# Kernel optimization log

Hardware: AMD Instinct MI355X
Metric: run time of the kernel (lower is better)

## Reference

```python
import jax, jax.numpy as jnp
import numpy as np

B, T, C = 4, 1024, 1024
H, HKV, D = 16, 4, 64
GATE_CH = 12
ROPE_THETA = 10000.0


def _rms_norm(x):
    # F.rms_norm with default eps = machine epsilon of dtype, no learnable scale
    eps = jnp.finfo(x.dtype).eps
    ms = jnp.mean(jnp.square(x), axis=-1, keepdims=True)
    return x * jax.lax.rsqrt(ms + eps)


def _apply_rotary(x, cos, sin):
    # x: (B, T, h, D); cos/sin: (1, T, 1, D//2). Half-split rotation.
    d = x.shape[-1] // 2
    x1, x2 = x[..., :d], x[..., d:]
    y1 = x1 * cos + x2 * sin
    y2 = -x1 * sin + x2 * cos
    return jnp.concatenate([y1, y2], axis=-1)


def setup_inputs() -> dict:
    key = jax.random.key(0)
    ks = jax.random.split(key, 8)
    x = jax.random.normal(ks[0], (B, T, C), dtype=jnp.float32)
    ve = jax.random.normal(ks[1], (B, T, HKV * D), dtype=jnp.float32)
    # real RoPE tables, shape (1, T, 1, D//2)
    half = D // 2
    inv_freq = 1.0 / (ROPE_THETA ** (np.arange(half, dtype=np.float32) / half))
    freqs = np.arange(T, dtype=np.float32)[:, None] * inv_freq[None, :]
    cos = jnp.asarray(np.cos(freqs), dtype=jnp.float32).reshape(1, T, 1, half)
    sin = jnp.asarray(np.sin(freqs), dtype=jnp.float32).reshape(1, T, 1, half)
    s = 0.02
    Wq = jax.random.normal(ks[2], (H * D, C), dtype=jnp.float32) * s
    Wk = jax.random.normal(ks[3], (HKV * D, C), dtype=jnp.float32) * s
    Wv = jax.random.normal(ks[4], (HKV * D, C), dtype=jnp.float32) * s
    Wo = jax.random.normal(ks[5], (C, C), dtype=jnp.float32) * s
    Wg = jax.random.normal(ks[6], (HKV, GATE_CH), dtype=jnp.float32) * s
    return {"x": x, "ve": ve, "cos": cos, "sin": sin,
            "Wq": Wq, "Wk": Wk, "Wv": Wv, "Wo": Wo, "Wg": Wg,
            "window_size": 256}


def reference(x, ve, cos, sin, Wq, Wk, Wv, Wo, Wg, window_size):
    b, t, c = x.shape
    d = 2 * cos.shape[-1]
    h = Wq.shape[0] // d
    hkv = Wk.shape[0] // d
    rep = h // hkv

    q = (x @ Wq.T).reshape(b, t, h, d)
    k = (x @ Wk.T).reshape(b, t, hkv, d)
    v = (x @ Wv.T).reshape(b, t, hkv, d)

    # value-embedding sigmoid gate (3 * sigmoid of first 12 channels of x)
    gate = 3.0 * jax.nn.sigmoid(x[..., : Wg.shape[1]] @ Wg.T)  # (b, t, hkv)
    v = v + gate[..., None] * ve.reshape(b, t, hkv, d)

    q = _apply_rotary(q, cos, sin)
    k = _apply_rotary(k, cos, sin)
    q = _rms_norm(q) * 1.2
    k = _rms_norm(k) * 1.2

    # GQA attention with sliding-window causal mask (left=window_size, right=0)
    qg = q.reshape(b, t, hkv, rep, d)
    scale = 1.0 / jnp.sqrt(jnp.asarray(d, dtype=q.dtype))
    scores = jnp.einsum('bqgrd,bkgd->bgrqk', qg, k) * scale
    i = jnp.arange(t)[:, None]
    j = jnp.arange(t)[None, :]
    mask = (j <= i) & ((i - j) <= window_size)  # (t, t)
    scores = jnp.where(mask[None, None, None], scores, -jnp.inf)
    probs = jax.nn.softmax(scores, axis=-1)
    y = jnp.einsum('bgrqk,bkgd->bqgrd', probs, v).reshape(b, t, h * d)
    return y @ Wo.T
```

## Files before the change

### kernel.cpp

```cpp
#include <hip/hip_runtime.h>

typedef __bf16 v8bf __attribute__((ext_vector_type(8)));
typedef float v4f __attribute__((ext_vector_type(4)));
typedef unsigned int v4u __attribute__((ext_vector_type(4)));
typedef unsigned int v2u __attribute__((ext_vector_type(2)));
typedef unsigned short u16;

#define DEVI static __device__ __forceinline__

DEVI float bf2f(u16 u) {
    union { float f; unsigned int i; } c; c.i = ((unsigned int)u) << 16; return c.f;
}
DEVI u16 f2bf(float f) {
    union { float f; unsigned int i; } c; c.f = f;
    unsigned int i = c.i;
    i += 0x7fffu + ((i >> 16) & 1u);
    return (u16)(i >> 16);
}

union Frag { v4u u; v8bf v; u16 h[8]; };

#define GLD16(gptr, lptr) __builtin_amdgcn_global_load_lds( \
    (const __attribute__((address_space(1))) void*)(gptr),  \
    (__attribute__((address_space(3))) void*)(lptr), 16, 0, 0)

__global__ __launch_bounds__(256) void convert5(
    const float* __restrict__ x, const float* __restrict__ wq,
    const float* __restrict__ wk, const float* __restrict__ wv,
    const float* __restrict__ wo, u16* __restrict__ xb,
    u16* __restrict__ wb, u16* __restrict__ wob)
{
    const float* src; u16* dst; int n;
    switch (blockIdx.y) {
        case 0: src = x;  dst = xb;               n = 4096 * 1024; break;
        case 1: src = wq; dst = wb;               n = 1024 * 1024; break;
        case 2: src = wk; dst = wb + 1024 * 1024; n = 256 * 1024;  break;
        case 3: src = wv; dst = wb + 1280 * 1024; n = 256 * 1024;  break;
        default: src = wo; dst = wob;             n = 1024 * 1024; break;
    }
    const int stride = gridDim.x * 256 * 4;
    for (int i = (blockIdx.x * 256 + threadIdx.x) * 4; i < n; i += stride) {
        const float4 f = *(const float4*)(src + i);
        v2u p;
        p[0] = (unsigned int)f2bf(f.x) | ((unsigned int)f2bf(f.y) << 16);
        p[1] = (unsigned int)f2bf(f.z) | ((unsigned int)f2bf(f.w) << 16);
        *(v2u*)(dst + i) = p;
    }
}

template <bool F32OUT>
__global__ __launch_bounds__(256) void gemm_bt(
    const u16* __restrict__ A, const u16* __restrict__ B,
    void* __restrict__ Cv, int N)
{
    __shared__ __align__(16) u16 As[64 * 32];
    __shared__ __align__(16) u16 Bs[128 * 32];
    const int tid  = threadIdx.x;
    const int lane = tid & 63, l15 = lane & 15, quad = lane >> 4;
    const int w    = tid >> 6;
    const int wr   = (w >> 1) * 32, wc = (w & 1) * 64;
    const int m0   = blockIdx.y * 64, n0 = blockIdx.x * 128;

    const u16* ab = A + m0 * 1024;
    const u16* bb = B + n0 * 1024;

    const int r0 = tid >> 2;
    const int c0 = (tid & 3) * 8;
    const u16* ag = ab + r0 * 1024 + c0;
    const u16* bg = bb + r0 * 1024 + c0;
    u16* al = &As[r0 * 32 + c0];
    u16* bl = &Bs[r0 * 32 + c0];

    v4f acc[2][4];
    const v4f vzero = {0.f, 0.f, 0.f, 0.f};
#pragma unroll
    for (int i = 0; i < 2; i++)
#pragma unroll
        for (int j = 0; j < 4; j++) acc[i][j] = vzero;

    for (int k0 = 0; k0 < 1024; k0 += 32) {
        __syncthreads();
        GLD16(ag + k0,             al);
        GLD16(bg + k0,             bl);
        GLD16(bg + k0 + 64 * 1024, bl + 64 * 32);
        __syncthreads();
        v8bf af[2];
#pragma unroll
        for (int mi = 0; mi < 2; mi++)
            af[mi] = *(const v8bf*)&As[(wr + mi * 16 + l15) * 32 + quad * 8];
#pragma unroll
        for (int ni = 0; ni < 4; ni++) {
            v8bf bv = *(const v8bf*)&Bs[(wc + ni * 16 + l15) * 32 + quad * 8];
#pragma unroll
            for (int mi = 0; mi < 2; mi++)
                acc[mi][ni] = __builtin_amdgcn_mfma_f32_16x16x32_bf16(af[mi], bv, acc[mi][ni], 0, 0, 0);
        }
    }
#pragma unroll
    for (int mi = 0; mi < 2; mi++) {
        const int row = m0 + wr + mi * 16 + quad * 4;
#pragma unroll
        for (int ni = 0; ni < 4; ni++) {
            const int col = n0 + wc + ni * 16 + l15;
#pragma unroll
            for (int r = 0; r < 4; r++) {
                if (F32OUT) ((float*)Cv)[(row + r) * N + col] = acc[mi][ni][r];
                else        ((u16*)Cv)[(row + r) * N + col] = f2bf(acc[mi][ni][r]);
            }
        }
    }
}

__global__ __launch_bounds__(256) void fixup(
    const u16* __restrict__ qkv, const float* __restrict__ x,
    const float* __restrict__ ve, const float* __restrict__ cs,
    const float* __restrict__ sn, const float* __restrict__ Wg,
    u16* __restrict__ qn, u16* __restrict__ kn, u16* __restrict__ vn)
{
    const int token = blockIdx.x;
    const int pos   = token & 1023;
    const int tid   = threadIdx.x;
    const int hw    = tid >> 5, l = tid & 31;
    const float c = cs[pos * 32 + l];
    const float s = sn[pos * 32 + l];
#pragma unroll
    for (int it = 0; it < 3; it++) {
        const int task = it * 8 + hw;
        if (task < 20) {
            const u16* src; u16* dst;
            if (task < 16) { src = qkv + token * 1536 + task * 64;               dst = qn + token * 1024 + task * 64; }
            else           { src = qkv + token * 1536 + 1024 + (task - 16) * 64; dst = kn + token * 256 + (task - 16) * 64; }
            const float x1 = bf2f(src[l]), x2 = bf2f(src[32 + l]);
            const float y1 = x1 * c + x2 * s;
            const float y2 = x2 * c - x1 * s;
            float ss = y1 * y1 + y2 * y2;
#pragma unroll
            for (int off = 16; off >= 1; off >>= 1) ss += __shfl_xor(ss, off, 64);
            const float inv = rsqrtf(ss * (1.0f / 64.0f) + 1.1920929e-7f) * 1.2f;
            dst[l]      = f2bf(y1 * inv);
            dst[32 + l] = f2bf(y2 * inv);
        } else {
            const int g = task - 20;
            float dot = 0.f;
#pragma unroll
            for (int cc = 0; cc < 12; cc++)
                dot += x[token * 1024 + cc] * Wg[g * 12 + cc];
            const float gate = 3.f / (1.f + __expf(-dot));
            const u16*   vsrc  = qkv + token * 1536 + 1280 + g * 64;
            const float* vesrc = ve + token * 256 + g * 64;
            u16* vdst = vn + token * 256 + g * 64;
            vdst[l]      = f2bf(bf2f(vsrc[l])      + gate * vesrc[l]);
            vdst[32 + l] = f2bf(bf2f(vsrc[32 + l]) + gate * vesrc[32 + l]);
        }
    }
}

__global__ __launch_bounds__(256) void attn(
    const u16* __restrict__ qn, const u16* __restrict__ kn,
    const u16* __restrict__ vn, u16* __restrict__ yo)
{
    __shared__ __align__(16) u16 Ks[64 * 72];
    __shared__ __align__(16) u16 VTs[64 * 72];
    __shared__ __align__(16) u16 Ps[4][16 * 72];
    const int tid  = threadIdx.x;
    const int w    = tid >> 6, lane = tid & 63, l15 = lane & 15, quad = lane >> 4;
    const int qb   = blockIdx.x, h = blockIdx.y, b = blockIdx.z;
    const int g    = h >> 2;
    const int qbase = qb * 64;
    const int qabs0 = qbase + w * 16;
    const int tok0  = b * 1024 + qabs0;
    u16* pw = Ps[w];

    v8bf qf[2];
#pragma unroll
    for (int ks = 0; ks < 2; ks++) {
        Frag f;
        f.u = *(const v4u*)&qn[(tok0 + l15) * 1024 + h * 64 + ks * 32 + quad * 8];
#pragma unroll
        for (int j = 0; j < 8; j++) f.h[j] = f2bf(0.125f * bf2f(f.h[j]));
        qf[ks] = f.v;
    }

    v4f o[4];
    float mi_[4], li_[4];
    const v4f vzero = {0.f, 0.f, 0.f, 0.f};
#pragma unroll
    for (int nd = 0; nd < 4; nd++) o[nd] = vzero;
#pragma unroll
    for (int r = 0; r < 4; r++) { mi_[r] = -1e30f; li_[r] = 0.f; }

    const int kstart = (qbase >= 256) ? qbase - 256 : 0;
    for (int kbase = kstart; kbase <= qbase; kbase += 64) {
        __syncthreads();
        {
            const int row = tid >> 2, ch = (tid & 3) * 16;
            const int goff = (b * 1024 + kbase + row) * 256 + g * 64 + ch;
            *(v4u*)&Ks[row * 72 + ch]     = *(const v4u*)&kn[goff];
            *(v4u*)&Ks[row * 72 + ch + 8] = *(const v4u*)&kn[goff + 8];
            Frag fv0; fv0.u = *(const v4u*)&vn[goff];
            Frag fv1; fv1.u = *(const v4u*)&vn[goff + 8];
#pragma unroll
            for (int j = 0; j < 8; j++) {
                VTs[(ch + j) * 72 + row]     = fv0.h[j];
                VTs[(ch + 8 + j) * 72 + row] = fv1.h[j];
            }
        }
        __syncthreads();

        bool skip[4], full[4];
#pragma unroll
        for (int ni = 0; ni < 4; ni++) {
            const int left = kbase + ni * 16;
            skip[ni] = (left > qabs0 + 15) || (qabs0 - (left + 15) > 256);
            full[ni] = ((left + 15) <= qabs0) && ((qabs0 + 15 - left) <= 256);
        }

        v4f sc[4];
        float rmax[4] = {-1e30f, -1e30f, -1e30f, -1e30f};
#pragma unroll
        for (int ni = 0; ni < 4; ni++) {
            if (skip[ni]) continue;
            v8bf kf0 = *(const v8bf*)&Ks[(ni * 16 + l15) * 72 + quad * 8];
            v8bf kf1 = *(const v8bf*)&Ks[(ni * 16 + l15) * 72 + 32 + quad * 8];
            v4f a = vzero;
            a = __builtin_amdgcn_mfma_f32_16x16x32_bf16(qf[0], kf0, a, 0, 0, 0);
            a = __builtin_amdgcn_mfma_f32_16x16x32_bf16(qf[1], kf1, a, 0, 0, 0);
            if (!full[ni]) {
                const int kj = kbase + ni * 16 + l15;
#pragma unroll
                for (int r = 0; r < 4; r++) {
                    const int qi = qabs0 + quad * 4 + r;
                    if (!((kj <= qi) && (qi - kj <= 256))) a[r] = -1e30f;
                }
            }
            sc[ni] = a;
#pragma unroll
            for (int r = 0; r < 4; r++) rmax[r] = fmaxf(rmax[r], a[r]);
        }
#pragma unroll
        for (int off = 8; off >= 1; off >>= 1)
#pragma unroll
            for (int r = 0; r < 4; r++)
                rmax[r] = fmaxf(rmax[r], __shfl_xor(rmax[r], off, 64));

        float mn[4], alp[4], ps[4];
#pragma unroll
        for (int r = 0; r < 4; r++) {
            mn[r]  = fmaxf(mi_[r], rmax[r]);
            alp[r] = __expf(mi_[r] - mn[r]);
            mi_[r] = mn[r];
            ps[r]  = 0.f;
        }
#pragma unroll
        for (int ni = 0; ni < 4; ni++) {
            if (skip[ni]) {
#pragma unroll
                for (int r = 0; r < 4; r++)
                    pw[(quad * 4 + r) * 72 + ni * 16 + l15] = 0;
            } else {
#pragma unroll
                for (int r = 0; r < 4; r++) {
                    const float p = __expf(sc[ni][r] - mn[r]);
                    ps[r] += p;
                    pw[(quad * 4 + r) * 72 + ni * 16 + l15] = f2bf(p);
                }
            }
        }
#pragma unroll
        for (int off = 8; off >= 1; off >>= 1)
#pragma unroll
            for (int r = 0; r < 4; r++)
                ps[r] += __shfl_xor(ps[r], off, 64);
#pragma unroll
        for (int r = 0; r < 4; r++)
            li_[r] = li_[r] * alp[r] + ps[r];
#pragma unroll
        for (int nd = 0; nd < 4; nd++)
#pragma unroll
            for (int r = 0; r < 4; r++)
                o[nd][r] *= alp[r];

#pragma unroll
        for (int ks = 0; ks < 2; ks++) {
            if (skip[2 * ks] && skip[2 * ks + 1]) continue;
            v8bf af = *(const v8bf*)&pw[l15 * 72 + ks * 32 + quad * 8];
#pragma unroll
            for (int nd = 0; nd < 4; nd++) {
                v8bf bv = *(const v8bf*)&VTs[(nd * 16 + l15) * 72 + ks * 32 + quad * 8];
                o[nd] = __builtin_amdgcn_mfma_f32_16x16x32_bf16(af, bv, o[nd], 0, 0, 0);
            }
        }
    }

    float inv[4];
#pragma unroll
    for (int r = 0; r < 4; r++) inv[r] = 1.f / li_[r];
#pragma unroll
    for (int nd = 0; nd < 4; nd++) {
        const int col = h * 64 + nd * 16 + l15;
#pragma unroll
        for (int r = 0; r < 4; r++) {
            const int row = tok0 + quad * 4 + r;
            yo[row * 1024 + col] = f2bf(o[nd][r] * inv[r]);
        }
    }
}

extern "C" void kernel_launch(void* const* d_in, const int* in_sizes, int n_in,
                              void* d_out, int out_size, void* d_ws, size_t ws_size,
                              hipStream_t stream)
{
    const float* x  = (const float*)d_in[0];
    const float* ve = (const float*)d_in[1];
    const float* cs = (const float*)d_in[2];
    const float* sn = (const float*)d_in[3];
    const float* Wq = (const float*)d_in[4];
    const float* Wk = (const float*)d_in[5];
    const float* Wv = (const float*)d_in[6];
    const float* Wo = (const float*)d_in[7];
    const float* Wg = (const float*)d_in[8];

    u16* xb  = (u16*)d_ws;
    u16* wb  = xb  + 4096 * 1024;
    u16* wob = wb  + 1536 * 1024;
    u16* qkv = wob + 1024 * 1024;
    u16* qn  = qkv + 4096 * 1536;
    u16* kn  = qn  + 4096 * 1024;
    u16* vn  = kn  + 4096 * 256;
    u16* ay  = qkv;

    convert5<<<dim3(512, 5), 256, 0, stream>>>(x, Wq, Wk, Wv, Wo, xb, wb, wob);
    gemm_bt<false><<<dim3(12, 64), 256, 0, stream>>>(xb, wb, (void*)qkv, 1536);
    fixup<<<4096, 256, 0, stream>>>(qkv, x, ve, cs, sn, Wg, qn, kn, vn);
    attn<<<dim3(16, 16, 4), 256, 0, stream>>>(qn, kn, vn, ay);
    gemm_bt<true><<<dim3(8, 64), 256, 0, stream>>>(ay, wob, d_out, 1024);
}
```

Before: 172.9 us.

## Pre-transpose V in a separate kernel and read K/V fragments directly from global

Adds a vtrans kernel that writes V transposed per (batch, kv-group) so that attention can load V^T MFMA fragments straight from global memory. The attention kernel drops its shared-memory K/V staging and both per-iteration __syncthreads, and reads K and V fragments directly from global/L2. This removes the scattered 2-byte LDS transpose stores and the block barriers. The cost is an extra kernel launch plus a pass over V, and K/V tiles are now fetched once per wave from cache instead of once per block.

```diff
diff --git a/kernel.cpp b/kernel.cpp
--- a/kernel.cpp
+++ b/kernel.cpp
@@ -155,12 +155,37 @@
     }
 }
 
+__global__ __launch_bounds__(256) void vtrans(
+    const u16* __restrict__ vn, u16* __restrict__ vt)
+{
+    __shared__ __align__(16) u16 T[64 * 72];
+    const int tid = threadIdx.x;
+    const int t0  = blockIdx.x * 64, g = blockIdx.y, b = blockIdx.z;
+    {
+        const int row = tid >> 2, ch = (tid & 3) * 16;
+        const int goff = (b * 1024 + t0 + row) * 256 + g * 64 + ch;
+        *(v4u*)&T[row * 72 + ch]     = *(const v4u*)&vn[goff];
+        *(v4u*)&T[row * 72 + ch + 8] = *(const v4u*)&vn[goff + 8];
+    }
+    __syncthreads();
+    {
+        const int d = tid >> 2, tc = (tid & 3) * 16;
+        Frag o0, o1;
+#pragma unroll
+        for (int j = 0; j < 8; j++) {
+            o0.h[j] = T[(tc + j) * 72 + d];
+            o1.h[j] = T[(tc + 8 + j) * 72 + d];
+        }
+        u16* dst = vt + ((b * 4 + g) * 64 + d) * 1024 + t0 + tc;
+        *(v4u*)dst       = o0.u;
+        *(v4u*)(dst + 8) = o1.u;
+    }
+}
+
 __global__ __launch_bounds__(256) void attn(
     const u16* __restrict__ qn, const u16* __restrict__ kn,
-    const u16* __restrict__ vn, u16* __restrict__ yo)
-{
-    __shared__ __align__(16) u16 Ks[64 * 72];
-    __shared__ __align__(16) u16 VTs[64 * 72];
+    const u16* __restrict__ vt, u16* __restrict__ yo)
+{
     __shared__ __align__(16) u16 Ps[4][16 * 72];
     const int tid  = threadIdx.x;
     const int w    = tid >> 6, lane = tid & 63, l15 = lane & 15, quad = lane >> 4;
@@ -171,6 +196,9 @@
     const int tok0  = b * 1024 + qabs0;
     u16* pw = Ps[w];
 
+    const u16* kbase_ptr = kn + (b * 1024) * 256 + g * 64;
+    const u16* vbase_ptr = vt + ((b * 4 + g) * 64) * 1024;
+
     v8bf qf[2];
 #pragma unroll
     for (int ks = 0; ks < 2; ks++) {
@@ -191,22 +219,6 @@
 
     const int kstart = (qbase >= 256) ? qbase - 256 : 0;
     for (int kbase = kstart; kbase <= qbase; kbase += 64) {
-        __syncthreads();
-        {
-            const int row = tid >> 2, ch = (tid & 3) * 16;
-            const int goff = (b * 1024 + kbase + row) * 256 + g * 64 + ch;
-            *(v4u*)&Ks[row * 72 + ch]     = *(const v4u*)&kn[goff];
-            *(v4u*)&Ks[row * 72 + ch + 8] = *(const v4u*)&kn[goff + 8];
-            Frag fv0; fv0.u = *(const v4u*)&vn[goff];
-            Frag fv1; fv1.u = *(const v4u*)&vn[goff + 8];
-#pragma unroll
-            for (int j = 0; j < 8; j++) {
-                VTs[(ch + j) * 72 + row]     = fv0.h[j];
-                VTs[(ch + 8 + j) * 72 + row] = fv1.h[j];
-            }
-        }
-        __syncthreads();
-
         bool skip[4], full[4];
 #pragma unroll
         for (int ni = 0; ni < 4; ni++) {
@@ -220,8 +232,9 @@
 #pragma unroll
         for (int ni = 0; ni < 4; ni++) {
             if (skip[ni]) continue;
-            v8bf kf0 = *(const v8bf*)&Ks[(ni * 16 + l15) * 72 + quad * 8];
-            v8bf kf1 = *(const v8bf*)&Ks[(ni * 16 + l15) * 72 + 32 + quad * 8];
+            const u16* kp = kbase_ptr + (kbase + ni * 16 + l15) * 256 + quad * 8;
+            v8bf kf0 = *(const v8bf*)kp;
+            v8bf kf1 = *(const v8bf*)(kp + 32);
             v4f a = vzero;
             a = __builtin_amdgcn_mfma_f32_16x16x32_bf16(qf[0], kf0, a, 0, 0, 0);
             a = __builtin_amdgcn_mfma_f32_16x16x32_bf16(qf[1], kf1, a, 0, 0, 0);
@@ -286,7 +299,7 @@
             v8bf af = *(const v8bf*)&pw[l15 * 72 + ks * 32 + quad * 8];
 #pragma unroll
             for (int nd = 0; nd < 4; nd++) {
-                v8bf bv = *(const v8bf*)&VTs[(nd * 16 + l15) * 72 + ks * 32 + quad * 8];
+                v8bf bv = *(const v8bf*)&vbase_ptr[(nd * 16 + l15) * 1024 + kbase + ks * 32 + quad * 8];
                 o[nd] = __builtin_amdgcn_mfma_f32_16x16x32_bf16(af, bv, o[nd], 0, 0, 0);
             }
         }
@@ -327,11 +340,13 @@
     u16* qn  = qkv + 4096 * 1536;
     u16* kn  = qn  + 4096 * 1024;
     u16* vn  = kn  + 4096 * 256;
+    u16* vt  = vn  + 4096 * 256;
     u16* ay  = qkv;
 
     convert5<<<dim3(512, 5), 256, 0, stream>>>(x, Wq, Wk, Wv, Wo, xb, wb, wob);
     gemm_bt<false><<<dim3(12, 64), 256, 0, stream>>>(xb, wb, (void*)qkv, 1536);
     fixup<<<4096, 256, 0, stream>>>(qkv, x, ve, cs, sn, Wg, qn, kn, vn);
-    attn<<<dim3(16, 16, 4), 256, 0, stream>>>(qn, kn, vn, ay);
+    vtrans<<<dim3(16, 4, 4), 256, 0, stream>>>(vn, vt);
+    attn<<<dim3(16, 16, 4), 256, 0, stream>>>(qn, kn, vt, ay);
     gemm_bt<true><<<dim3(8, 64), 256, 0, stream>>>(ay, wob, d_out, 1024);
 }
```

Result: slower. 185.4 us (+7.2%).
